# Performance work log

Hardware: AMD Instinct MI355X
Metric: run time of the kernel (lower is better)

## Reference

```python
import jax, jax.numpy as jnp
import numpy as np

EPS = 1e-5


def _conv(x, w, padding=0, dilation=1, groups=1):
    return jax.lax.conv_general_dilated(
        x, w, window_strides=(1, 1),
        padding=[(padding, padding), (padding, padding)],
        rhs_dilation=(dilation, dilation),
        dimension_numbers=('NCHW', 'OIHW', 'NCHW'),
        feature_group_count=groups)


def _bn(x, gamma, beta, mean, var):
    # eval-mode BatchNorm2d over channel dim (NCHW)
    scale = (gamma * jax.lax.rsqrt(var + EPS))[None, :, None, None]
    shift = (beta - mean * gamma * jax.lax.rsqrt(var + EPS))[None, :, None, None]
    return x * scale + shift


def setup_inputs() -> dict:
    key = jax.random.key(0)
    B, Cin, H, W = 16, 256, 64, 64
    Chid, Cout = 256, 256
    ks = [3, 5, 7, 9]
    keys = jax.random.split(key, 32)
    ki = iter(keys)

    def rn(shape, scale=0.05):
        return jax.random.normal(next(ki), shape, dtype=jnp.float32) * scale

    inp = {'x': jax.random.normal(next(ki), (B, Cin, H, W), dtype=jnp.float32)}
    # pre_conv: 1x1 conv (no bias) + BN + ReLU
    inp['pre_w'] = rn((Chid, Cin, 1, 1))
    inp['bn1_g'] = 1.0 + rn((Chid,))
    inp['bn1_b'] = rn((Chid,))
    inp['bn1_m'] = rn((Chid,))
    inp['bn1_v'] = jnp.abs(1.0 + rn((Chid,)))
    # depthwise convs k=3,5,7,9 (bias, no BN)
    for k in ks:
        inp[f'dw{k}_w'] = rn((Chid, 1, k, k))
        inp[f'dw{k}_b'] = rn((Chid,))
    # pw_conv: 1x1 + BN + ReLU
    inp['pw_w'] = rn((Chid, Chid, 1, 1))
    inp['bn2_g'] = 1.0 + rn((Chid,))
    inp['bn2_b'] = rn((Chid,))
    inp['bn2_m'] = rn((Chid,))
    inp['bn2_v'] = jnp.abs(1.0 + rn((Chid,)))
    # post_conv: 1x1 + BN + ReLU
    inp['post_w'] = rn((Cout, Chid, 1, 1))
    inp['bn3_g'] = 1.0 + rn((Cout,))
    inp['bn3_b'] = rn((Cout,))
    inp['bn3_m'] = rn((Cout,))
    inp['bn3_v'] = jnp.abs(1.0 + rn((Cout,)))
    return inp


def reference(x, pre_w, bn1_g, bn1_b, bn1_m, bn1_v,
              dw3_w, dw3_b, dw5_w, dw5_b, dw7_w, dw7_b, dw9_w, dw9_b,
              pw_w, bn2_g, bn2_b, bn2_m, bn2_v,
              post_w, bn3_g, bn3_b, bn3_m, bn3_v):
    C = pre_w.shape[0]
    # pre_conv
    h = jax.nn.relu(_bn(_conv(x, pre_w), bn1_g, bn1_b, bn1_m, bn1_v))
    # sum of identity + 4 depthwise branches (same-padded)
    s = h
    for k, w, b in ((3, dw3_w, dw3_b), (5, dw5_w, dw5_b),
                    (7, dw7_w, dw7_b), (9, dw9_w, dw9_b)):
        s = s + _conv(h, w, padding=(k - 1) // 2, groups=C) + b[None, :, None, None]
    # pw_conv then post_conv
    s = jax.nn.relu(_bn(_conv(s, pw_w), bn2_g, bn2_b, bn2_m, bn2_v))
    out = jax.nn.relu(_bn(_conv(s, post_w), bn3_g, bn3_b, bn3_m, bn3_v))
    return out
```

## Files before the change

kernel.cpp:

```cpp
#include <hip/hip_runtime.h>
#include <stdint.h>

#define HW 4096
#define CCH 256
#define BPL (CCH * HW)
#define LSTR 264

typedef __attribute__((ext_vector_type(8))) short short8;
typedef __attribute__((ext_vector_type(4))) float floatx4;
typedef unsigned short ushort_t;

__device__ inline ushort_t f2bf(float f) {
    union { float f; unsigned int u; } v; v.f = f;
    unsigned int r = v.u + 0x7FFFu + ((v.u >> 16) & 1u);
    return (ushort_t)(r >> 16);
}
__device__ inline float bf2f(ushort_t u) {
    union { unsigned int u; float f; } v; v.u = ((unsigned int)u) << 16;
    return v.f;
}

__global__ void prep_kernel(
    const float* __restrict__ pre_w, const float* __restrict__ pw_w, const float* __restrict__ post_w,
    const float* __restrict__ g1, const float* __restrict__ b1, const float* __restrict__ m1, const float* __restrict__ v1,
    const float* __restrict__ g2, const float* __restrict__ b2, const float* __restrict__ m2, const float* __restrict__ v2,
    const float* __restrict__ g3, const float* __restrict__ b3, const float* __restrict__ m3, const float* __restrict__ v3,
    const float* __restrict__ w3d, const float* __restrict__ b3d,
    const float* __restrict__ w5d, const float* __restrict__ b5d,
    const float* __restrict__ w7d, const float* __restrict__ b7d,
    const float* __restrict__ w9d, const float* __restrict__ b9d,
    ushort_t* __restrict__ w1b, ushort_t* __restrict__ w2b, ushort_t* __restrict__ w3b,
    float* __restrict__ WcP, float* __restrict__ biasc,
    float* __restrict__ sc1, float* __restrict__ sh1,
    float* __restrict__ sc2, float* __restrict__ sh2,
    float* __restrict__ sc3, float* __restrict__ sh3)
{
    int c = blockIdx.x, t = threadIdx.x;
    w1b[c * 256 + t] = f2bf(pre_w[c * 256 + t]);
    w2b[c * 256 + t] = f2bf(pw_w[c * 256 + t]);
    w3b[c * 256 + t] = f2bf(post_w[c * 256 + t]);
    if (t < 128) {
        float val = 0.f;
        int dy = -1, dx = 0;
        if (t < 45) { dy = t / 9; dx = t % 9; }
        else if (t >= 64 && t < 100) { int i = t - 64; dy = 5 + i / 9; dx = i % 9; }
        if (dy >= 0) {
            val = w9d[c * 81 + dy * 9 + dx];
            if (dy >= 1 && dy <= 7 && dx >= 1 && dx <= 7) val += w7d[c * 49 + (dy - 1) * 7 + (dx - 1)];
            if (dy >= 2 && dy <= 6 && dx >= 2 && dx <= 6) val += w5d[c * 25 + (dy - 2) * 5 + (dx - 2)];
            if (dy >= 3 && dy <= 5 && dx >= 3 && dx <= 5) val += w3d[c * 9 + (dy - 3) * 3 + (dx - 3)];
            if (dy == 4 && dx == 4) val += 1.0f;
        }
        WcP[c * 128 + t] = val;
    }
    if (t == 128) { float s = g1[c] * rsqrtf(v1[c] + 1e-5f); sc1[c] = s; sh1[c] = b1[c] - m1[c] * s; }
    if (t == 129) { float s = g2[c] * rsqrtf(v2[c] + 1e-5f); sc2[c] = s; sh2[c] = b2[c] - m2[c] * s; }
    if (t == 130) { float s = g3[c] * rsqrtf(v3[c] + 1e-5f); sc3[c] = s; sh3[c] = b3[c] - m3[c] * s; }
    if (t == 131) biasc[c] = b3d[c] + b5d[c] + b7d[c] + b9d[c];
}

template <int MODE>
__global__ __launch_bounds__(256, 2) void conv_tile(
    const void* __restrict__ inp,
    const ushort_t* __restrict__ wA, const float* __restrict__ scA, const float* __restrict__ shA,
    const ushort_t* __restrict__ wB, const float* __restrict__ scB, const float* __restrict__ shB,
    void* __restrict__ outp)
{
    __shared__ __align__(16) ushort_t Bs[128 * LSTR];
    const int tid = threadIdx.x;
    const int P0 = blockIdx.x * 128;
    const int b = P0 >> 12, hw0 = P0 & 4095;
    unsigned int* Bsd = (unsigned int*)Bs;

    {
        const int c2 = tid & 127, ph = tid >> 7, px0 = ph * 64;
        if (MODE == 0) {
            const float* s0 = (const float*)inp + (size_t)b * BPL + (size_t)(2 * c2) * HW + hw0 + px0;
            const float* s1 = s0 + HW;
#pragma unroll
            for (int i = 0; i < 16; i++) {
                float4 v0 = *(const float4*)(s0 + 4 * i);
                float4 v1 = *(const float4*)(s1 + 4 * i);
                const int px = px0 + 4 * i;
                Bsd[(px + 0) * (LSTR / 2) + c2] = (unsigned)f2bf(v0.x) | ((unsigned)f2bf(v1.x) << 16);
                Bsd[(px + 1) * (LSTR / 2) + c2] = (unsigned)f2bf(v0.y) | ((unsigned)f2bf(v1.y) << 16);
                Bsd[(px + 2) * (LSTR / 2) + c2] = (unsigned)f2bf(v0.z) | ((unsigned)f2bf(v1.z) << 16);
                Bsd[(px + 3) * (LSTR / 2) + c2] = (unsigned)f2bf(v0.w) | ((unsigned)f2bf(v1.w) << 16);
            }
        } else {
            const ushort_t* s0 = (const ushort_t*)inp + (size_t)b * BPL + (size_t)(2 * c2) * HW + hw0 + px0;
            const ushort_t* s1 = s0 + HW;
#pragma unroll
            for (int i = 0; i < 8; i++) {
                union { uint4 v; ushort_t u[8]; } r0, r1;
                r0.v = *(const uint4*)(s0 + 8 * i);
                r1.v = *(const uint4*)(s1 + 8 * i);
                const int px = px0 + 8 * i;
#pragma unroll
                for (int j = 0; j < 8; j++)
                    Bsd[(px + j) * (LSTR / 2) + c2] = (unsigned)r0.u[j] | ((unsigned)r1.u[j] << 16);
            }
        }
    }
    __syncthreads();

    const int wave = tid >> 6, lane = tid & 63, quad = lane >> 4, L = lane & 15;
    const int coutw = wave * 64;

    floatx4 acc[4][8];

    auto run_gemm = [&](const ushort_t* W) {
#pragma unroll
        for (int mt = 0; mt < 4; mt++)
#pragma unroll
            for (int nt = 0; nt < 8; nt++) acc[mt][nt] = (floatx4){0.f, 0.f, 0.f, 0.f};
        const ushort_t* Ab = W + (size_t)(coutw + L) * CCH + quad * 8;
        short8 Ac[4], An[4];
#pragma unroll
        for (int mt = 0; mt < 4; mt++) Ac[mt] = *(const short8*)(Ab + mt * 16 * CCH);
#pragma unroll
        for (int kt = 0; kt < 8; kt++) {
            if (kt < 7) {
#pragma unroll
                for (int mt = 0; mt < 4; mt++)
                    An[mt] = *(const short8*)(Ab + mt * 16 * CCH + (kt + 1) * 32);
            }
            short8 Bf[8];
#pragma unroll
            for (int nt = 0; nt < 8; nt++)
                Bf[nt] = *(const short8*)&Bs[(nt * 16 + L) * LSTR + kt * 32 + quad * 8];
#pragma unroll
            for (int mt = 0; mt < 4; mt++)
#pragma unroll
                for (int nt = 0; nt < 8; nt++)
                    acc[mt][nt] = __builtin_amdgcn_mfma_f32_16x16x32_bf16(
                        Ac[mt], Bf[nt], acc[mt][nt], 0, 0, 0);
            if (kt < 7) {
#pragma unroll
                for (int mt = 0; mt < 4; mt++) Ac[mt] = An[mt];
            }
        }
    };

    run_gemm(wA);

    if (MODE == 0) {
        ushort_t* outb = (ushort_t*)outp + (size_t)b * BPL + hw0;
#pragma unroll
        for (int mt = 0; mt < 4; mt++) {
#pragma unroll
            for (int r = 0; r < 4; r++) {
                const int cout = coutw + mt * 16 + quad * 4 + r;
                const float s = scA[cout], h0 = shA[cout];
#pragma unroll
                for (int nt = 0; nt < 8; nt++)
                    outb[(size_t)cout * HW + nt * 16 + L] =
                        f2bf(fmaxf(fmaf(acc[mt][nt][r], s, h0), 0.f));
            }
        }
    } else {
        __syncthreads();
#pragma unroll
        for (int mt = 0; mt < 4; mt++) {
            const int cout0 = coutw + mt * 16 + quad * 4;
            float sc4[4], sh4[4];
#pragma unroll
            for (int r = 0; r < 4; r++) { sc4[r] = scA[cout0 + r]; sh4[r] = shA[cout0 + r]; }
#pragma unroll
            for (int nt = 0; nt < 8; nt++) {
                const int px = nt * 16 + L;
                ushort4 pk;
                pk.x = f2bf(fmaxf(fmaf(acc[mt][nt][0], sc4[0], sh4[0]), 0.f));
                pk.y = f2bf(fmaxf(fmaf(acc[mt][nt][1], sc4[1], sh4[1]), 0.f));
                pk.z = f2bf(fmaxf(fmaf(acc[mt][nt][2], sc4[2], sh4[2]), 0.f));
                pk.w = f2bf(fmaxf(fmaf(acc[mt][nt][3], sc4[3], sh4[3]), 0.f));
                *(ushort4*)&Bs[px * LSTR + cout0] = pk;
            }
        }
        __syncthreads();
        run_gemm(wB);
        float* outb = (float*)outp + (size_t)b * BPL + hw0;
#pragma unroll
        for (int mt = 0; mt < 4; mt++) {
#pragma unroll
            for (int r = 0; r < 4; r++) {
                const int cout = coutw + mt * 16 + quad * 4 + r;
                const float s = scB[cout], h0 = shB[cout];
#pragma unroll
                for (int nt = 0; nt < 8; nt++)
                    outb[(size_t)cout * HW + nt * 16 + L] =
                        fmaxf(fmaf(acc[mt][nt][r], s, h0), 0.f);
            }
        }
    }
}

__global__ __launch_bounds__(256, 3) void dw_kernel(
    const ushort_t* __restrict__ h, const float* __restrict__ WcP,
    const float* __restrict__ biasc, ushort_t* __restrict__ out)
{
    const int bcp = blockIdx.x, c = bcp & 255;
    const size_t plane = (size_t)bcp * HW;
    __shared__ float tile[72 * 72];
    const int tid = threadIdx.x;

    for (int f = tid; f < 272; f += 256) {
        int row, col4;
        if (f < 144) { int r = f / 18; row = (r < 4) ? r : r + 64; col4 = (f % 18) * 4; }
        else { int f2 = f - 144; row = 4 + (f2 >> 1); col4 = (f2 & 1) ? 68 : 0; }
        *(float4*)&tile[row * 72 + col4] = (float4){0.f, 0.f, 0.f, 0.f};
    }
    {
        const int r = tid >> 2, q = tid & 3;
        const ushort_t* src = h + plane + r * 64 + q * 16;
        union { uint4 v; ushort_t u[8]; } a, bq;
        a.v  = *(const uint4*)src;
        bq.v = *(const uint4*)(src + 8);
        float* drow = &tile[(r + 4) * 72 + 4 + q * 16];
        float4 t0, t1;
        t0.x = bf2f(a.u[0]); t0.y = bf2f(a.u[1]); t0.z = bf2f(a.u[2]); t0.w = bf2f(a.u[3]);
        t1.x = bf2f(a.u[4]); t1.y = bf2f(a.u[5]); t1.z = bf2f(a.u[6]); t1.w = bf2f(a.u[7]);
        *(float4*)&drow[0] = t0; *(float4*)&drow[4] = t1;
        t0.x = bf2f(bq.u[0]); t0.y = bf2f(bq.u[1]); t0.z = bf2f(bq.u[2]); t0.w = bf2f(bq.u[3]);
        t1.x = bf2f(bq.u[4]); t1.y = bf2f(bq.u[5]); t1.z = bf2f(bq.u[6]); t1.w = bf2f(bq.u[7]);
        *(float4*)&drow[8] = t0; *(float4*)&drow[12] = t1;
    }
    __syncthreads();

    const int tx = tid & 15, ty = tid >> 4;
    const int x0 = tx * 4, y0 = ty * 4;
    float acc[4][4];
#pragma unroll
    for (int i = 0; i < 4; i++)
#pragma unroll
        for (int j = 0; j < 4; j++) acc[i][j] = 0.f;

    const float* wp = WcP + c * 128;
    float wr[48];

#pragma unroll
    for (int i = 0; i < 12; i++) *(float4*)&wr[4 * i] = *(const float4*)(wp + 4 * i);
#pragma unroll
    for (int r6 = 0; r6 < 8; r6++) {
        const float* row = &tile[(y0 + r6) * 72 + x0];
        float win[12];
        *(float4*)&win[0] = *(const float4*)&row[0];
        *(float4*)&win[4] = *(const float4*)&row[4];
        *(float4*)&win[8] = *(const float4*)&row[8];
#pragma unroll
        for (int yy = 0; yy < 4; yy++) {
            const int d = r6 - yy;
            if (d >= 0 && d <= 4) {
#pragma unroll
                for (int t = 0; t < 9; t++)
#pragma unroll
                    for (int j = 0; j < 4; j++)
                        acc[yy][j] = fmaf(wr[d * 9 + t], win[j + t], acc[yy][j]);
            }
        }
    }
#pragma unroll
    for (int i = 0; i < 9; i++) *(float4*)&wr[4 * i] = *(const float4*)(wp + 64 + 4 * i);
#pragma unroll
    for (int r6 = 5; r6 < 12; r6++) {
        const float* row = &tile[(y0 + r6) * 72 + x0];
        float win[12];
        *(float4*)&win[0] = *(const float4*)&row[0];
        *(float4*)&win[4] = *(const float4*)&row[4];
        *(float4*)&win[8] = *(const float4*)&row[8];
#pragma unroll
        for (int yy = 0; yy < 4; yy++) {
            const int d = r6 - yy;
            if (d >= 5 && d <= 8) {
#pragma unroll
                for (int t = 0; t < 9; t++)
#pragma unroll
                    for (int j = 0; j < 4; j++)
                        acc[yy][j] = fmaf(wr[(d - 5) * 9 + t], win[j + t], acc[yy][j]);
            }
        }
    }

    const float bb = biasc[c];
#pragma unroll
    for (int yy = 0; yy < 4; yy++) {
        ushort4 o;
        o.x = f2bf(acc[yy][0] + bb);
        o.y = f2bf(acc[yy][1] + bb);
        o.z = f2bf(acc[yy][2] + bb);
        o.w = f2bf(acc[yy][3] + bb);
        *(ushort4*)&out[plane + (size_t)(y0 + yy) * 64 + x0] = o;
    }
}

extern "C" void kernel_launch(void* const* d_in, const int* in_sizes, int n_in,
                              void* d_out, int out_size, void* d_ws, size_t ws_size,
                              hipStream_t stream) {
    const float* x     = (const float*)d_in[0];
    const float* pre_w = (const float*)d_in[1];
    const float* bn1g  = (const float*)d_in[2];
    const float* bn1b  = (const float*)d_in[3];
    const float* bn1m  = (const float*)d_in[4];
    const float* bn1v  = (const float*)d_in[5];
    const float* dw3w  = (const float*)d_in[6];
    const float* dw3b  = (const float*)d_in[7];
    const float* dw5w  = (const float*)d_in[8];
    const float* dw5b  = (const float*)d_in[9];
    const float* dw7w  = (const float*)d_in[10];
    const float* dw7b  = (const float*)d_in[11];
    const float* dw9w  = (const float*)d_in[12];
    const float* dw9b  = (const float*)d_in[13];
    const float* pww   = (const float*)d_in[14];
    const float* bn2g  = (const float*)d_in[15];
    const float* bn2b  = (const float*)d_in[16];
    const float* bn2m  = (const float*)d_in[17];
    const float* bn2v  = (const float*)d_in[18];
    const float* postw = (const float*)d_in[19];
    const float* bn3g  = (const float*)d_in[20];
    const float* bn3b  = (const float*)d_in[21];
    const float* bn3m  = (const float*)d_in[22];
    const float* bn3v  = (const float*)d_in[23];

    char* wsb = (char*)d_ws;
    ushort_t* sbuf = (ushort_t*)wsb;
    ushort_t* hbuf = (ushort_t*)d_out;
    char* aux = wsb + (size_t)33 * 1024 * 1024;
    ushort_t* w1b = (ushort_t*)aux;
    ushort_t* w2b = w1b + 65536;
    ushort_t* w3b = w2b + 65536;
    float* WcP   = (float*)(w3b + 65536);
    float* biasc = WcP + 256 * 128;
    float* sc1 = biasc + 256;  float* sh1 = sc1 + 256;
    float* sc2 = sh1 + 256;    float* sh2 = sc2 + 256;
    float* sc3 = sh2 + 256;    float* sh3 = sc3 + 256;

    prep_kernel<<<256, 256, 0, stream>>>(
        pre_w, pww, postw,
        bn1g, bn1b, bn1m, bn1v, bn2g, bn2b, bn2m, bn2v, bn3g, bn3b, bn3m, bn3v,
        dw3w, dw3b, dw5w, dw5b, dw7w, dw7b, dw9w, dw9b,
        w1b, w2b, w3b, WcP, biasc, sc1, sh1, sc2, sh2, sc3, sh3);

    conv_tile<0><<<512, 256, 0, stream>>>(x, w1b, sc1, sh1,
                                          nullptr, nullptr, nullptr, hbuf);
    dw_kernel<<<16 * CCH, 256, 0, stream>>>(hbuf, WcP, biasc, sbuf);
    conv_tile<1><<<512, 256, 0, stream>>>(sbuf, w2b, sc2, sh2,
                                          w3b, sc3, sh3, (float*)d_out);
}
```

Baseline: 244.1 us.

## Halve GEMM pixel tile for more blocks; store depthwise tile as bf16

The 1x1-conv GEMM kernels now process 64 pixels per block instead of 128. The launch doubles to 1024 blocks, the accumulator array is halved, and launch bounds are raised to 3 blocks per SM, which should improve occupancy and load balance across CUs. The depthwise kernel keeps its halo tile in LDS as packed bf16 instead of fp32 and unpacks to float when reading the windows. That halves shared-memory footprint and write traffic at the cost of extra unpack ALU work. The smaller GEMM tiles reuse each weight fragment across fewer pixels, so weight loads per MFMA roughly double.

```diff
diff --git a/kernel.cpp b/kernel.cpp
--- a/kernel.cpp
+++ b/kernel.cpp
@@ -15,9 +15,11 @@
     unsigned int r = v.u + 0x7FFFu + ((v.u >> 16) & 1u);
     return (ushort_t)(r >> 16);
 }
-__device__ inline float bf2f(ushort_t u) {
-    union { unsigned int u; float f; } v; v.u = ((unsigned int)u) << 16;
-    return v.f;
+__device__ inline float bflo(unsigned u) {
+    union { unsigned u; float f; } v; v.u = u << 16; return v.f;
+}
+__device__ inline float bfhi(unsigned u) {
+    union { unsigned u; float f; } v; v.u = u & 0xFFFF0000u; return v.f;
 }
 
 __global__ void prep_kernel(
@@ -60,25 +62,25 @@
 }
 
 template <int MODE>
-__global__ __launch_bounds__(256, 2) void conv_tile(
+__global__ __launch_bounds__(256, 3) void conv_tile(
     const void* __restrict__ inp,
     const ushort_t* __restrict__ wA, const float* __restrict__ scA, const float* __restrict__ shA,
     const ushort_t* __restrict__ wB, const float* __restrict__ scB, const float* __restrict__ shB,
     void* __restrict__ outp)
 {
-    __shared__ __align__(16) ushort_t Bs[128 * LSTR];
+    __shared__ __align__(16) ushort_t Bs[64 * LSTR];
     const int tid = threadIdx.x;
-    const int P0 = blockIdx.x * 128;
+    const int P0 = blockIdx.x * 64;
     const int b = P0 >> 12, hw0 = P0 & 4095;
     unsigned int* Bsd = (unsigned int*)Bs;
 
     {
-        const int c2 = tid & 127, ph = tid >> 7, px0 = ph * 64;
+        const int c2 = tid & 127, ph = tid >> 7, px0 = ph * 32;
         if (MODE == 0) {
             const float* s0 = (const float*)inp + (size_t)b * BPL + (size_t)(2 * c2) * HW + hw0 + px0;
             const float* s1 = s0 + HW;
 #pragma unroll
-            for (int i = 0; i < 16; i++) {
+            for (int i = 0; i < 8; i++) {
                 float4 v0 = *(const float4*)(s0 + 4 * i);
                 float4 v1 = *(const float4*)(s1 + 4 * i);
                 const int px = px0 + 4 * i;
@@ -91,7 +93,7 @@
             const ushort_t* s0 = (const ushort_t*)inp + (size_t)b * BPL + (size_t)(2 * c2) * HW + hw0 + px0;
             const ushort_t* s1 = s0 + HW;
 #pragma unroll
-            for (int i = 0; i < 8; i++) {
+            for (int i = 0; i < 4; i++) {
                 union { uint4 v; ushort_t u[8]; } r0, r1;
                 r0.v = *(const uint4*)(s0 + 8 * i);
                 r1.v = *(const uint4*)(s1 + 8 * i);
@@ -107,13 +109,13 @@
     const int wave = tid >> 6, lane = tid & 63, quad = lane >> 4, L = lane & 15;
     const int coutw = wave * 64;
 
-    floatx4 acc[4][8];
+    floatx4 acc[4][4];
 
     auto run_gemm = [&](const ushort_t* W) {
 #pragma unroll
         for (int mt = 0; mt < 4; mt++)
 #pragma unroll
-            for (int nt = 0; nt < 8; nt++) acc[mt][nt] = (floatx4){0.f, 0.f, 0.f, 0.f};
+            for (int nt = 0; nt < 4; nt++) acc[mt][nt] = (floatx4){0.f, 0.f, 0.f, 0.f};
         const ushort_t* Ab = W + (size_t)(coutw + L) * CCH + quad * 8;
         short8 Ac[4], An[4];
 #pragma unroll
@@ -125,14 +127,14 @@
                 for (int mt = 0; mt < 4; mt++)
                     An[mt] = *(const short8*)(Ab + mt * 16 * CCH + (kt + 1) * 32);
             }
-            short8 Bf[8];
-#pragma unroll
-            for (int nt = 0; nt < 8; nt++)
+            short8 Bf[4];
+#pragma unroll
+            for (int nt = 0; nt < 4; nt++)
                 Bf[nt] = *(const short8*)&Bs[(nt * 16 + L) * LSTR + kt * 32 + quad * 8];
 #pragma unroll
             for (int mt = 0; mt < 4; mt++)
 #pragma unroll
-                for (int nt = 0; nt < 8; nt++)
+                for (int nt = 0; nt < 4; nt++)
                     acc[mt][nt] = __builtin_amdgcn_mfma_f32_16x16x32_bf16(
                         Ac[mt], Bf[nt], acc[mt][nt], 0, 0, 0);
             if (kt < 7) {
@@ -153,7 +155,7 @@
                 const int cout = coutw + mt * 16 + quad * 4 + r;
                 const float s = scA[cout], h0 = shA[cout];
 #pragma unroll
-                for (int nt = 0; nt < 8; nt++)
+                for (int nt = 0; nt < 4; nt++)
                     outb[(size_t)cout * HW + nt * 16 + L] =
                         f2bf(fmaxf(fmaf(acc[mt][nt][r], s, h0), 0.f));
             }
@@ -167,7 +169,7 @@
 #pragma unroll
             for (int r = 0; r < 4; r++) { sc4[r] = scA[cout0 + r]; sh4[r] = shA[cout0 + r]; }
 #pragma unroll
-            for (int nt = 0; nt < 8; nt++) {
+            for (int nt = 0; nt < 4; nt++) {
                 const int px = nt * 16 + L;
                 ushort4 pk;
                 pk.x = f2bf(fmaxf(fmaf(acc[mt][nt][0], sc4[0], sh4[0]), 0.f));
@@ -187,7 +189,7 @@
                 const int cout = coutw + mt * 16 + quad * 4 + r;
                 const float s = scB[cout], h0 = shB[cout];
 #pragma unroll
-                for (int nt = 0; nt < 8; nt++)
+                for (int nt = 0; nt < 4; nt++)
                     outb[(size_t)cout * HW + nt * 16 + L] =
                         fmaxf(fmaf(acc[mt][nt][r], s, h0), 0.f);
             }
@@ -201,29 +203,26 @@
 {
     const int bcp = blockIdx.x, c = bcp & 255;
     const size_t plane = (size_t)bcp * HW;
-    __shared__ float tile[72 * 72];
+    __shared__ __align__(16) ushort_t tile[72 * 72];
+    unsigned* td = (unsigned*)tile;
     const int tid = threadIdx.x;
 
-    for (int f = tid; f < 272; f += 256) {
-        int row, col4;
-        if (f < 144) { int r = f / 18; row = (r < 4) ? r : r + 64; col4 = (f % 18) * 4; }
-        else { int f2 = f - 144; row = 4 + (f2 >> 1); col4 = (f2 & 1) ? 68 : 0; }
-        *(float4*)&tile[row * 72 + col4] = (float4){0.f, 0.f, 0.f, 0.f};
+    for (int f = tid; f < 544; f += 256) {
+        int row, col;
+        if (f < 288) { row = f / 36; if (row >= 4) row += 64; col = f % 36; }
+        else { int f2 = f - 288; row = 4 + (f2 >> 2); int k = f2 & 3; col = (k < 2) ? k : 32 + k; }
+        td[row * 36 + col] = 0u;
     }
     {
         const int r = tid >> 2, q = tid & 3;
         const ushort_t* src = h + plane + r * 64 + q * 16;
-        union { uint4 v; ushort_t u[8]; } a, bq;
-        a.v  = *(const uint4*)src;
-        bq.v = *(const uint4*)(src + 8);
-        float* drow = &tile[(r + 4) * 72 + 4 + q * 16];
-        float4 t0, t1;
-        t0.x = bf2f(a.u[0]); t0.y = bf2f(a.u[1]); t0.z = bf2f(a.u[2]); t0.w = bf2f(a.u[3]);
-        t1.x = bf2f(a.u[4]); t1.y = bf2f(a.u[5]); t1.z = bf2f(a.u[6]); t1.w = bf2f(a.u[7]);
-        *(float4*)&drow[0] = t0; *(float4*)&drow[4] = t1;
-        t0.x = bf2f(bq.u[0]); t0.y = bf2f(bq.u[1]); t0.z = bf2f(bq.u[2]); t0.w = bf2f(bq.u[3]);
-        t1.x = bf2f(bq.u[4]); t1.y = bf2f(bq.u[5]); t1.z = bf2f(bq.u[6]); t1.w = bf2f(bq.u[7]);
-        *(float4*)&drow[8] = t0; *(float4*)&drow[12] = t1;
+        uint4 a = *(const uint4*)src;
+        uint4 bq = *(const uint4*)(src + 8);
+        uint2* dst = (uint2*)(td + (r + 4) * 36 + 2 + q * 8);
+        dst[0] = make_uint2(a.x, a.y);
+        dst[1] = make_uint2(a.z, a.w);
+        dst[2] = make_uint2(bq.x, bq.y);
+        dst[3] = make_uint2(bq.z, bq.w);
     }
     __syncthreads();
 
@@ -242,11 +241,14 @@
     for (int i = 0; i < 12; i++) *(float4*)&wr[4 * i] = *(const float4*)(wp + 4 * i);
 #pragma unroll
     for (int r6 = 0; r6 < 8; r6++) {
-        const float* row = &tile[(y0 + r6) * 72 + x0];
+        const ushort_t* rowp = &tile[(y0 + r6) * 72 + x0];
+        uint2 a0 = *(const uint2*)rowp;
+        uint2 a1 = *(const uint2*)(rowp + 4);
+        uint2 a2 = *(const uint2*)(rowp + 8);
         float win[12];
-        *(float4*)&win[0] = *(const float4*)&row[0];
-        *(float4*)&win[4] = *(const float4*)&row[4];
-        *(float4*)&win[8] = *(const float4*)&row[8];
+        win[0] = bflo(a0.x); win[1] = bfhi(a0.x); win[2]  = bflo(a0.y); win[3]  = bfhi(a0.y);
+        win[4] = bflo(a1.x); win[5] = bfhi(a1.x); win[6]  = bflo(a1.y); win[7]  = bfhi(a1.y);
+        win[8] = bflo(a2.x); win[9] = bfhi(a2.x); win[10] = bflo(a2.y); win[11] = bfhi(a2.y);
 #pragma unroll
         for (int yy = 0; yy < 4; yy++) {
             const int d = r6 - yy;
@@ -263,11 +265,14 @@
     for (int i = 0; i < 9; i++) *(float4*)&wr[4 * i] = *(const float4*)(wp + 64 + 4 * i);
 #pragma unroll
     for (int r6 = 5; r6 < 12; r6++) {
-        const float* row = &tile[(y0 + r6) * 72 + x0];
+        const ushort_t* rowp = &tile[(y0 + r6) * 72 + x0];
+        uint2 a0 = *(const uint2*)rowp;
+        uint2 a1 = *(const uint2*)(rowp + 4);
+        uint2 a2 = *(const uint2*)(rowp + 8);
         float win[12];
-        *(float4*)&win[0] = *(const float4*)&row[0];
-        *(float4*)&win[4] = *(const float4*)&row[4];
-        *(float4*)&win[8] = *(const float4*)&row[8];
+        win[0] = bflo(a0.x); win[1] = bfhi(a0.x); win[2]  = bflo(a0.y); win[3]  = bfhi(a0.y);
+        win[4] = bflo(a1.x); win[5] = bfhi(a1.x); win[6]  = bflo(a1.y); win[7]  = bfhi(a1.y);
+        win[8] = bflo(a2.x); win[9] = bfhi(a2.x); win[10] = bflo(a2.y); win[11] = bfhi(a2.y);
 #pragma unroll
         for (int yy = 0; yy < 4; yy++) {
             const int d = r6 - yy;
@@ -340,9 +345,9 @@
         dw3w, dw3b, dw5w, dw5b, dw7w, dw7b, dw9w, dw9b,
         w1b, w2b, w3b, WcP, biasc, sc1, sh1, sc2, sh2, sc3, sh3);
 
-    conv_tile<0><<<512, 256, 0, stream>>>(x, w1b, sc1, sh1,
-                                          nullptr, nullptr, nullptr, hbuf);
+    conv_tile<0><<<1024, 256, 0, stream>>>(x, w1b, sc1, sh1,
+                                           nullptr, nullptr, nullptr, hbuf);
     dw_kernel<<<16 * CCH, 256, 0, stream>>>(hbuf, WcP, biasc, sbuf);
-    conv_tile<1><<<512, 256, 0, stream>>>(sbuf, w2b, sc2, sh2,
-                                          w3b, sc3, sh3, (float*)d_out);
-}
+    conv_tile<1><<<1024, 256, 0, stream>>>(sbuf, w2b, sc2, sh2,
+                                           w3b, sc3, sh3, (float*)d_out);
+}
```

Result: slower. 259.3 us (+6.2%).
